# Performance work log

Hardware: AMD Instinct MI355X
Metric: run time of the kernel (lower is better)

## Reference

```python
import jax, jax.numpy as jnp
import numpy as np

KH, KW = 3, 3
STRIDE, PAD = 2, 1
NEG_SLOPE = 0.2
EPS = 1e-5


def conv2d(x, w, stride, pad):
    return jax.lax.conv_general_dilated(
        x, w, window_strides=(stride, stride),
        padding=[(pad, pad), (pad, pad)],
        dimension_numbers=('NCHW', 'OIHW', 'NCHW'))


def deform_conv2d(x, offsets, w_def):
    # x: [B,C,H,W]; offsets: [B,2*K,Ho,Wo] (per-kernel-tap (dy,dx) pairs);
    # w_def: [Cout,Cin,KH,KW]. Matches torchvision DeformConv2d (v1, no mask).
    B, C, H, W = x.shape
    Ho, Wo = offsets.shape[2], offsets.shape[3]
    K = KH * KW
    off = offsets.reshape(B, K, 2, Ho, Wo)
    dy, dx = off[:, :, 0], off[:, :, 1]            # [B,K,Ho,Wo]

    ky = jnp.arange(KH).repeat(KW).astype(x.dtype)   # [K]
    kx = jnp.tile(jnp.arange(KW), KH).astype(x.dtype)
    base_y = (jnp.arange(Ho) * STRIDE - PAD).astype(x.dtype)  # [Ho]
    base_x = (jnp.arange(Wo) * STRIDE - PAD).astype(x.dtype)

    # sampling positions [B,K,Ho,Wo]
    py = base_y[None, None, :, None] + ky[None, :, None, None] + dy
    px = base_x[None, None, None, :] + kx[None, :, None, None] + dx

    y0f = jnp.floor(py); x0f = jnp.floor(px)
    wy1 = py - y0f; wy0 = 1.0 - wy1
    wx1 = px - x0f; wx0 = 1.0 - wx1
    y0 = y0f.astype(jnp.int32); x0 = x0f.astype(jnp.int32)
    y1 = y0 + 1; x1 = x0 + 1

    xt = jnp.transpose(x, (0, 2, 3, 1))  # [B,H,W,C] for channel-last gather
    bidx = jnp.arange(B)[:, None, None, None]

    def corner(yi, xi):
        valid = ((yi >= 0) & (yi < H) & (xi >= 0) & (xi < W)).astype(x.dtype)
        yc = jnp.clip(yi, 0, H - 1); xc = jnp.clip(xi, 0, W - 1)
        v = xt[bidx, yc, xc]                         # [B,K,Ho,Wo,C]
        return v * valid[..., None]

    sampled = (corner(y0, x0) * (wy0 * wx0)[..., None]
               + corner(y0, x1) * (wy0 * wx1)[..., None]
               + corner(y1, x0) * (wy1 * wx0)[..., None]
               + corner(y1, x1) * (wy1 * wx1)[..., None])  # [B,K,Ho,Wo,C]

    wk = w_def.reshape(w_def.shape[0], w_def.shape[1], K)   # [Cout,Cin,K]
    return jnp.einsum('bkhwc,ock->bohw', sampled, wk)


def leaky_relu(x):
    return jnp.where(x >= 0, x, NEG_SLOPE * x)


def instance_norm(x):
    mean = jnp.mean(x, axis=(2, 3), keepdims=True)
    var = jnp.var(x, axis=(2, 3), keepdims=True)
    return (x - mean) * jax.lax.rsqrt(var + EPS)


def setup_inputs() -> dict:
    key = jax.random.key(0)
    k1, k2, k3, k4 = jax.random.split(key, 4)
    B, Cin, H, W = 8, 256, 128, 128
    Cout = 256
    x = jax.random.normal(k1, (B, Cin, H, W), dtype=jnp.float32)
    # conv_offset weight: predicts 2*K offset channels
    w_off = jax.random.normal(k2, (2 * KH * KW, Cin, KH, KW), dtype=jnp.float32) * 0.01
    w_def = jax.random.normal(k3, (Cout, Cin, KH, KW), dtype=jnp.float32) * 0.02
    w_1x1 = jax.random.normal(k4, (Cout, Cout, 1, 1), dtype=jnp.float32) * 0.02
    return {"x": x, "w_off": w_off, "w_def": w_def, "w_1x1": w_1x1}


def reference(x, w_off, w_def, w_1x1):
    offsets = conv2d(x, w_off, STRIDE, PAD)          # [B,18,Ho,Wo]
    y = deform_conv2d(x, offsets, w_def)             # [B,Cout,Ho,Wo]
    y = leaky_relu(y)
    y = conv2d(y, w_1x1, 1, 0)
    y = instance_norm(y)
    return leaky_relu(y)
```

## Files before the change

### kernel.cpp

```cpp
#include <hip/hip_runtime.h>

#define B_   8
#define CIN  256
#define H_   128
#define W_   128
#define HO   64
#define WO   64
#define CO_  256
#define NEG  0.2f

typedef __attribute__((ext_vector_type(8))) _Float16 h16x8;
typedef __attribute__((ext_vector_type(4))) float f32x4;
typedef unsigned short u16;

#define OFF_OFS   0
#define WDEF_OFS  589824
#define W1_OFS    884736
#define WBOFF_OFS 917504
#define Y1_OFS    954368
#define XBF_OFS   5148672
#define TAP_OFS   21925888
#define WS_NEED_TAP ((21925888ull + 1179648ull) * 4ull)

__device__ __forceinline__ float lrelu(float v) { return v >= 0.f ? v : NEG * v; }

__device__ __forceinline__ u16 f2h(float f) {
    _Float16 h = (_Float16)f;
    return *(u16*)&h;
}

__device__ __forceinline__ void gld16(const void* g, void* l) {
    __builtin_amdgcn_global_load_lds((const __attribute__((address_space(1))) unsigned*)g,
                                     (__attribute__((address_space(3))) unsigned*)l, 16, 0, 0);
}

__global__ __launch_bounds__(256) void prep(
    const float* __restrict__ wdef, const float* __restrict__ w1,
    const float* __restrict__ woff,
    u16* __restrict__ wdefh, u16* __restrict__ w1h, u16* __restrict__ wboff)
{
    int i = blockIdx.x * 256 + threadIdx.x;
    if (i < 9 * 256 * 256) {
        int c  = i & 255;
        int co = (i >> 8) & 255;
        int k  = i >> 16;
        wdefh[i] = f2h(wdef[((size_t)co * 256 + c) * 9 + k]);
    }
    if (i < 65536) w1h[i] = f2h(w1[i]);
    if (i < 73728) {
        int j  = i & 7;
        int s  = (i >> 3) & 7;
        int co = (i >> 6) & 31;
        int ch = (i >> 11) & 3;
        int k  = i >> 13;
        int c  = ch * 64 + ((s ^ ((co >> 1) & 7)) << 3) + j;
        wboff[i] = (co < 18) ? f2h(woff[((size_t)co * 256 + c) * 9 + k]) : (u16)0;
    }
}

__global__ __launch_bounds__(256) void nchw2nhwc(
    const float* __restrict__ x, u16* __restrict__ xh)
{
    __shared__ float tile[64][128];
    int bid = blockIdx.x;
    int g = bid & 3;
    int y = (bid >> 2) & 127;
    int b = bid >> 9;
    int t = threadIdx.x;

    const float* src = x + ((size_t)(b * 256 + g * 64) * 128 + y) * 128;
#pragma unroll
    for (int p = 0; p < 8; ++p) {
        int i = p * 256 + t;
        int cc = i >> 5, x4 = (i & 31) * 4;
        *(float4*)&tile[cc][x4] = *(const float4*)(src + (size_t)cc * 16384 + x4);
    }
    __syncthreads();

    int xpos = t >> 1, h = t & 1;
    u16 buf[32];
#pragma unroll
    for (int j = 0; j < 32; ++j) buf[j] = f2h(tile[h * 32 + j][xpos]);
    u16* dst = xh + (((size_t)b * 128 + y) * 128 + xpos) * 256 + g * 64 + h * 32;
#pragma unroll
    for (int q = 0; q < 4; ++q)
        *(int4*)(dst + q * 8) = *(int4*)(buf + q * 8);
}

__global__ __launch_bounds__(256) void offconv_mfma(
    const u16* __restrict__ xh, const u16* __restrict__ wboff,
    float* __restrict__ off, int4* __restrict__ tap)
{
    __shared__ __align__(16) char smem[57728];
    u16* xrowU = (u16*)smem;
    u16* bU    = (u16*)(smem + 49536);

    int blk = blockIdx.x;
    blk = (blk & 7) * 64 + (blk >> 3);
    int b = blk >> 6, ho = blk & 63;
    int t = threadIdx.x;
    int lane = t & 63, w = t >> 6;
    int r = lane & 15, kg = lane >> 4;

    const u16* xB = xh + (size_t)b * (128 * 128 * 256);

    f32x4 acc[2];
    acc[0] = f32x4{0.f, 0.f, 0.f, 0.f};
    acc[1] = f32x4{0.f, 0.f, 0.f, 0.f};

    if (t < 24) {
        int ry = t >> 3, s = t & 7;
        *(int4*)(smem + (ry * 129 * 8 + s) * 16) = int4{0, 0, 0, 0};
    }

    for (int ch = 0; ch < 4; ++ch) {
        __syncthreads();
        for (int ry = 0; ry < 3; ++ry) {
            int y = 2 * ho - 1 + ry;
            int rowbase = (ry * 129 + 1) * 128;
            if ((unsigned)y < 128u) {
#pragma unroll
                for (int p = 0; p < 4; ++p) {
                    int u = p * 256 + t;
                    int xpi = u >> 3, s = u & 7;
                    int c8 = s ^ (((xpi + 1) >> 1) & 7);
                    gld16(xB + ((size_t)(y * 128 + xpi)) * 256 + ch * 64 + c8 * 8,
                          smem + rowbase + p * 4096 + w * 1024);
                }
            } else if (ch == 0) {
#pragma unroll
                for (int p = 0; p < 4; ++p)
                    *(int4*)(smem + rowbase + (p * 256 + t) * 16) = int4{0, 0, 0, 0};
            }
        }
        gld16(wboff + (size_t)(0 * 4 + ch) * 2048 + t * 8,
              smem + 49536 + w * 1024);
        __syncthreads();

        for (int k = 0; k < 9; ++k) {
            int buf = k & 1;
            if (k < 8)
                gld16(wboff + (size_t)((k + 1) * 4 + ch) * 2048 + t * 8,
                      smem + 49536 + (buf ^ 1) * 4096 + w * 1024);
            int ky = k / 3, kx = k - 3 * ky;
            int pixA = w * 16 + r;
            int xp = 2 * pixA + kx;
            int abase = (ky * 129 + xp) * 64;
            int swA = (xp >> 1) & 7;
#pragma unroll
            for (int ksub = 0; ksub < 2; ++ksub) {
                int lc = ksub * 4 + kg;
                h16x8 a = *(h16x8*)(xrowU + abase + ((lc ^ swA) << 3));
#pragma unroll
                for (int n = 0; n < 2; ++n) {
                    int co = n * 16 + r;
                    h16x8 bb = *(h16x8*)(bU + buf * 2048 + co * 64 +
                                         ((lc ^ ((co >> 1) & 7)) << 3));
                    acc[n] = __builtin_amdgcn_mfma_f32_16x16x32_f16(a, bb, acc[n], 0, 0, 0);
                }
            }
            __syncthreads();
        }
    }

    float* offL = (float*)smem;
#pragma unroll
    for (int n = 0; n < 2; ++n) {
        int co = n * 16 + r;
        if (co < 18) {
#pragma unroll
            for (int j = 0; j < 4; ++j) {
                int wo = w * 16 + kg * 4 + j;
                float v = acc[n][j];
                off[(((size_t)b * 18 + co) * 64 + ho) * 64 + wo] = v;
                offL[co * 64 + wo] = v;
            }
        }
    }
    if (tap) {
        __syncthreads();
        for (int i = t; i < 576; i += 256) {
            int pix = i / 9, k = i - 9 * (i / 9);
            int ky = k / 3, kx = k - 3 * ky;
            float dy = offL[(2 * k) * 64 + pix];
            float dx = offL[(2 * k + 1) * 64 + pix];
            float py = (float)(ho * 2 - 1 + ky) + dy;
            float px = (float)(pix * 2 - 1 + kx) + dx;
            float y0f = floorf(py), x0f = floorf(px);
            int y0 = (int)y0f, x0i = (int)x0f;
            float wy1 = py - y0f, wx1 = px - x0f;
            float wy0 = 1.f - wy1, wx0 = 1.f - wx1;
            int y1i = y0 + 1, x1i = x0i + 1;
            bool vy0 = (unsigned)y0  < 128u;
            bool vy1 = (unsigned)y1i < 128u;
            bool vx0 = (unsigned)x0i < 128u;
            bool vx1 = (unsigned)x1i < 128u;
            int yc0 = min(max(y0, 0), 127), yc1 = min(max(y1i, 0), 127);
            int xc0 = min(max(x0i, 0), 127), xc1 = min(max(x1i, 0), 127);
            int4 e;
            e.x = (yc0 * 128 + xc0) * 512 | (xc1 - xc0) | ((yc1 - yc0) << 1);
            e.y = (int)((unsigned)f2h((vy0 && vx0) ? wy0 * wx0 : 0.f) |
                        ((unsigned)f2h((vy0 && vx1) ? wy0 * wx1 : 0.f) << 16));
            e.z = (int)((unsigned)f2h((vy1 && vx0) ? wy1 * wx0 : 0.f) |
                        ((unsigned)f2h((vy1 && vx1) ? wy1 * wx1 : 0.f) << 16));
            e.w = 0;
            tap[(size_t)(b * 64 + ho) * 576 + i] = e;
        }
    }
}

__global__ __launch_bounds__(512, 4) void deform_fused(
    const u16* __restrict__ xh, const int4* __restrict__ tap,
    const u16* __restrict__ wdefh, const u16* __restrict__ w1h,
    float* __restrict__ out)
{
    extern __shared__ __align__(16) char smem[];

    int blk = blockIdx.x;
    blk = (blk & 7) * 64 + (blk >> 3);
    int b = blk >> 6, ho = blk & 63;
    int t = threadIdx.x;
    int lane = t & 63, w = t >> 6;
    int r = lane & 15, kg = lane >> 4;
    int pixS = w * 8 + (lane >> 3);
    int cs   = lane & 7;

    f32x4 acc[4][2];
    f32x4 zz = {0.f, 0.f, 0.f, 0.f};
#pragma unroll
    for (int m = 0; m < 4; ++m)
#pragma unroll
        for (int n = 0; n < 2; ++n) acc[m][n] = zz;

    const int4* tapB = tap + (size_t)(b * 64 + ho) * 576 + pixS * 9;
    const char* xb2  = (const char*)(xh + (size_t)b * (128 * 128 * 256)) + cs * 16;

    int sbw = pixS * 128 + ((cs ^ (pixS & 7)) << 4);

    auto stage = [&](int k, int ch, int dbuf) {
        const u16* wk = wdefh + ((size_t)k << 16);
#pragma unroll
        for (int p2 = 0; p2 < 4; ++p2) {
            int i = p2 * 512 + t;
            int co = i >> 3, s = i & 7;
            gld16(wk + (size_t)co * 256 + ch * 64 + ((s ^ (co & 7)) << 3),
                  smem + dbuf * 32768 + p2 * 8192 + w * 1024);
        }
    };

    {
        stage(0, 0, 0);
        int4 e = tapB[0];
        int o00 = e.x & 0x7FFFFE00;
        int dxo = (e.x & 1) << 9;
        int dyo = (e.x & 2) << 15;
        h16x8 c00 = *(const h16x8*)(xb2 + o00);
        h16x8 c01 = *(const h16x8*)(xb2 + o00 + dxo);
        h16x8 c10 = *(const h16x8*)(xb2 + o00 + dyo);
        h16x8 c11 = *(const h16x8*)(xb2 + o00 + dyo + dxo);
        union U { int u; _Float16 h[2]; };
        U u01, u23;
        u01.u = e.y; u23.u = e.z;
        h16x8 v = c00 * u01.h[0] + c01 * u01.h[1] + c10 * u23.h[0] + c11 * u23.h[1];
        *(h16x8*)(smem + 65536 + sbw) = v;
    }
    __syncthreads();

    for (int p = 0; p < 36; ++p) {
        int cur = p & 1;
        bool nx = p < 35;
        int4 e;
        h16x8 c00, c01, c10, c11;
        if (nx) {
            int pn = p + 1;
            int chn = pn / 9, kn = pn - 9 * chn;
            e = tapB[kn];
            int o00 = e.x & 0x7FFFFE00;
            int dxo = (e.x & 1) << 9;
            int dyo = (e.x & 2) << 15;
            const char* base = xb2 + chn * 128;
            c00 = *(const h16x8*)(base + o00);
            c01 = *(const h16x8*)(base + o00 + dxo);
            c10 = *(const h16x8*)(base + o00 + dyo);
            c11 = *(const h16x8*)(base + o00 + dyo + dxo);
            stage(kn, chn, cur ^ 1);
        }
        {
            u16* wb = (u16*)(smem + cur * 32768);
            u16* sb = (u16*)(smem + 65536 + cur * 8192);
            h16x8 af[4], bfr[2];
            __builtin_amdgcn_s_setprio(1);
#pragma unroll
            for (int ksub = 0; ksub < 2; ++ksub) {
                int so = ((ksub * 4 + kg) ^ (r & 7)) << 3;
#pragma unroll
                for (int m = 0; m < 4; ++m)
                    af[m] = *(h16x8*)(sb + (m * 16 + r) * 64 + so);
#pragma unroll
                for (int n = 0; n < 2; ++n)
                    bfr[n] = *(h16x8*)(wb + (w * 32 + n * 16 + r) * 64 + so);
#pragma unroll
                for (int m = 0; m < 4; ++m)
#pragma unroll
                    for (int n = 0; n < 2; ++n)
                        acc[m][n] = __builtin_amdgcn_mfma_f32_16x16x32_f16(af[m], bfr[n], acc[m][n], 0, 0, 0);
            }
            __builtin_amdgcn_s_setprio(0);
        }
        if (nx) {
            union U { int u; _Float16 h[2]; };
            U u01, u23;
            u01.u = e.y; u23.u = e.z;
            h16x8 v = c00 * u01.h[0] + c01 * u01.h[1] + c10 * u23.h[0] + c11 * u23.h[1];
            *(h16x8*)(smem + 65536 + (cur ^ 1) * 8192 + sbw) = v;
        }
        __syncthreads();
    }

    char* outT = smem + 32768;
    int rg = lane >> 4;
#pragma unroll
    for (int m = 0; m < 4; ++m)
#pragma unroll
        for (int n = 0; n < 2; ++n) {
            int co = w * 32 + n * 16 + r;
#pragma unroll
            for (int j = 0; j < 4; ++j) {
                int prow = m * 16 + rg * 4 + j;
                *(u16*)(outT + prow * 512 + ((co * 2) ^ ((prow & 7) << 4))) =
                    f2h(lrelu(acc[m][n][j]));
            }
        }

    auto stage1 = [&](int ch2) {
#pragma unroll
        for (int p2 = 0; p2 < 4; ++p2) {
            int i = p2 * 512 + t;
            int o = i >> 3, s = i & 7;
            gld16(w1h + (size_t)o * 256 + ch2 * 64 + ((s ^ (o & 7)) << 3),
                  smem + p2 * 8192 + w * 1024);
        }
    };

    stage1(0);
#pragma unroll
    for (int m = 0; m < 4; ++m)
#pragma unroll
        for (int n = 0; n < 2; ++n) acc[m][n] = zz;
    __syncthreads();

    for (int ch2 = 0; ch2 < 4; ++ch2) {
        h16x8 af[4], bfr[2];
        __builtin_amdgcn_s_setprio(1);
#pragma unroll
        for (int ksub = 0; ksub < 2; ++ksub) {
            int cb = (ch2 * 64 + (ksub * 4 + kg) * 8) * 2;
#pragma unroll
            for (int m = 0; m < 4; ++m) {
                int prow = m * 16 + r;
                af[m] = *(h16x8*)(outT + prow * 512 + (cb ^ ((prow & 7) << 4)));
            }
#pragma unroll
            for (int n = 0; n < 2; ++n) {
                int o = w * 32 + n * 16 + r;
                bfr[n] = *(h16x8*)(smem + o * 128 + (((ksub * 4 + kg) ^ (o & 7)) << 4));
            }
#pragma unroll
            for (int m = 0; m < 4; ++m)
#pragma unroll
                for (int n = 0; n < 2; ++n)
                    acc[m][n] = __builtin_amdgcn_mfma_f32_16x16x32_f16(af[m], bfr[n], acc[m][n], 0, 0, 0);
        }
        __builtin_amdgcn_s_setprio(0);
        __syncthreads();
        if (ch2 < 3) {
            stage1(ch2 + 1);
            __syncthreads();
        }
    }

#pragma unroll
    for (int m = 0; m < 4; ++m)
#pragma unroll
        for (int n = 0; n < 2; ++n) {
            int o = w * 32 + n * 16 + r;
            int pix0 = m * 16 + rg * 4;
            float4 v;
            v.x = acc[m][n][0]; v.y = acc[m][n][1];
            v.z = acc[m][n][2]; v.w = acc[m][n][3];
            *(float4*)(out + ((size_t)(b * 256 + o) * 64 + ho) * 64 + pix0) = v;
        }
}

__global__ __launch_bounds__(512, 4) void deform_inline(
    const u16* __restrict__ xh, const float* __restrict__ off,
    const u16* __restrict__ wdefh, u16* __restrict__ y1p)
{
    extern __shared__ __align__(16) char smem[];

    int blk = blockIdx.x;
    blk = (blk & 7) * 64 + (blk >> 3);
    int b = blk >> 6, ho = blk & 63;
    int t = threadIdx.x;
    int lane = t & 63, w = t >> 6;
    int r = lane & 15, kg = lane >> 4;
    int pixS = w * 8 + (lane >> 3);
    int cs   = lane & 7;

    f32x4 acc[4][2];
    f32x4 zz = {0.f, 0.f, 0.f, 0.f};
#pragma unroll
    for (int m = 0; m < 4; ++m)
#pragma unroll
        for (int n = 0; n < 2; ++n) acc[m][n] = zz;

    const u16* xB = xh + (size_t)b * (128 * 128 * 256);

    int o00, o01, o10, o11;
    float f00, f01, f10, f11;

    auto coords = [&](int k) {
        int ky = k / 3, kx = k - 3 * ky;
        float dy = off[(((size_t)b * 18 + 2 * k    ) * 64 + ho) * 64 + pixS];
        float dx = off[(((size_t)b * 18 + 2 * k + 1) * 64 + ho) * 64 + pixS];
        float py = (float)(ho * 2 - 1 + ky) + dy;
        float px = (float)(pixS * 2 - 1 + kx) + dx;
        float y0f = floorf(py), x0f = floorf(px);
        int y0 = (int)y0f, x0i = (int)x0f;
        float wy1 = py - y0f, wx1 = px - x0f;
        float wy0 = 1.f - wy1, wx0 = 1.f - wx1;
        int y1i = y0 + 1, x1i = x0i + 1;
        bool vy0 = (unsigned)y0  < 128u;
        bool vy1 = (unsigned)y1i < 128u;
        bool vx0 = (unsigned)x0i < 128u;
        bool vx1 = (unsigned)x1i < 128u;
        int yc0 = min(max(y0, 0), 127), yc1 = min(max(y1i, 0), 127);
        int xc0 = min(max(x0i, 0), 127), xc1 = min(max(x1i, 0), 127);
        o00 = yc0 * 128 + xc0;  o01 = yc0 * 128 + xc1;
        o10 = yc1 * 128 + xc0;  o11 = yc1 * 128 + xc1;
        f00 = (vy0 && vx0) ? wy0 * wx0 : 0.f;
        f01 = (vy0 && vx1) ? wy0 * wx1 : 0.f;
        f10 = (vy1 && vx0) ? wy1 * wx0 : 0.f;
        f11 = (vy1 && vx1) ? wy1 * wx1 : 0.f;
    };

    auto stage = [&](int k, int ch, int dbuf) {
        const u16* wk = wdefh + ((size_t)k << 16);
#pragma unroll
        for (int p2 = 0; p2 < 4; ++p2) {
            int i = p2 * 512 + t;
            int co = i >> 3, s = i & 7;
            gld16(wk + (size_t)co * 256 + ch * 64 + ((s ^ (co & 7)) << 3),
                  smem + dbuf * 32768 + p2 * 8192 + w * 1024);
        }
    };

    auto sample = [&](int ch, int dbuf) {
        int cw = ch * 64 + cs * 8;
        const u16* q00 = xB + (size_t)o00 * 256 + cw;
        const u16* q01 = xB + (size_t)o01 * 256 + cw;
        const u16* q10 = xB + (size_t)o10 * 256 + cw;
        const u16* q11 = xB + (size_t)o11 * 256 + cw;
        h16x8 c00 = *(const h16x8*)q00;
        h16x8 c01 = *(const h16x8*)q01;
        h16x8 c10 = *(const h16x8*)q10;
        h16x8 c11 = *(const h16x8*)q11;
        _Float16 hf00 = (_Float16)f00, hf01 = (_Float16)f01;
        _Float16 hf10 = (_Float16)f10, hf11 = (_Float16)f11;
        h16x8 v = c00 * hf00 + c01 * hf01 + c10 * hf10 + c11 * hf11;
        *(h16x8*)(smem + 65536 + dbuf * 8192 + pixS * 128 + ((cs ^ (pixS & 7)) << 4)) = v;
    };

    coords(0);
    stage(0, 0, 0);
    sample(0, 0);
    __syncthreads();

    for (int p = 0; p < 36; ++p) {
        int cur = p & 1;
        if (p < 35) {
            int pn = p + 1;
            int chn = pn / 9, kn = pn - 9 * chn;
            stage(kn, chn, cur ^ 1);
            coords(kn);
            sample(chn, cur ^ 1);
        }
        u16* wb = (u16*)(smem + cur * 32768);
        u16* sb = (u16*)(smem + 65536 + cur * 8192);
        h16x8 af[4], bfr[2];
        __builtin_amdgcn_s_setprio(1);
#pragma unroll
        for (int ksub = 0; ksub < 2; ++ksub) {
            int so = ((ksub * 4 + kg) ^ (r & 7)) << 3;
#pragma unroll
            for (int m = 0; m < 4; ++m)
                af[m] = *(h16x8*)(sb + (m * 16 + r) * 64 + so);
#pragma unroll
            for (int n = 0; n < 2; ++n)
                bfr[n] = *(h16x8*)(wb + (w * 32 + n * 16 + r) * 64 + so);
#pragma unroll
            for (int m = 0; m < 4; ++m)
#pragma unroll
                for (int n = 0; n < 2; ++n)
                    acc[m][n] = __builtin_amdgcn_mfma_f32_16x16x32_f16(af[m], bfr[n], acc[m][n], 0, 0, 0);
        }
        __builtin_amdgcn_s_setprio(0);
        __syncthreads();
    }

    u16* outT = (u16*)smem;
    int rg = lane >> 4;
#pragma unroll
    for (int m = 0; m < 4; ++m)
#pragma unroll
        for (int n = 0; n < 2; ++n) {
            int co = w * 32 + n * 16 + r;
#pragma unroll
            for (int j = 0; j < 4; ++j) {
                int prow = m * 16 + rg * 4 + j;
                outT[prow * 256 + co] = f2h(lrelu(acc[m][n][j]));
            }
        }
    __syncthreads();
    u16* dst = y1p + (size_t)(b * 64 + ho) * 16384;
#pragma unroll
    for (int p = 0; p < 4; ++p)
        *(int4*)((char*)dst + p * 8192 + t * 16) = *(int4*)(smem + p * 8192 + t * 16);
}

__global__ __launch_bounds__(256) void conv1x1_mfma(
    const u16* __restrict__ y1p, const u16* __restrict__ w1h,
    float* __restrict__ out)
{
    __shared__ __align__(16) char smem[20480];
    u16* btile = (u16*)smem;
    u16* atile = (u16*)(smem + 16384);

    int blk = blockIdx.x;
    blk = (blk & 7) * 64 + (blk >> 3);
    int b = blk >> 6, ho = blk & 63;
    int t = threadIdx.x, lane = t & 63, w = t >> 6;
    int r = lane & 15, kg = lane >> 4;
    int sR = (r >> 1) & 3;

    f32x4 acc[4][4];
    f32x4 zz = {0.f, 0.f, 0.f, 0.f};
#pragma unroll
    for (int m = 0; m < 4; ++m)
#pragma unroll
        for (int n = 0; n < 4; ++n) acc[m][n] = zz;

    const u16* abase = y1p + (size_t)(b * 64 + ho) * 16384;

    for (int ch = 0; ch < 8; ++ch) {
#pragma unroll
        for (int p = 0; p < 4; ++p) {
            int slot = p * 256 + t;
            int o = slot >> 2, qq = slot & 3;
            gld16(w1h + o * 256 + ch * 32 + ((qq ^ ((o >> 1) & 3)) << 3),
                  smem + p * 4096 + (t >> 6) * 1024);
        }
        {
            int pix = t >> 2, qq = t & 3;
            gld16(abase + pix * 256 + ch * 32 + ((qq ^ ((pix >> 1) & 3)) << 3),
                  smem + 16384 + (t >> 6) * 1024);
        }
        __syncthreads();
        h16x8 af[4], bfr[4];
#pragma unroll
        for (int m = 0; m < 4; ++m)
            af[m] = *(h16x8*)(atile + (m * 16 + r) * 32 + ((kg ^ sR) << 3));
#pragma unroll
        for (int n = 0; n < 4; ++n)
            bfr[n] = *(h16x8*)(btile + (w * 64 + n * 16 + r) * 32 + ((kg ^ sR) << 3));
#pragma unroll
        for (int m = 0; m < 4; ++m)
#pragma unroll
            for (int n = 0; n < 4; ++n)
                acc[m][n] = __builtin_amdgcn_mfma_f32_16x16x32_f16(af[m], bfr[n], acc[m][n], 0, 0, 0);
        __syncthreads();
    }

    int rg = lane >> 4;
#pragma unroll
    for (int m = 0; m < 4; ++m)
#pragma unroll
        for (int n = 0; n < 4; ++n) {
            int o = w * 64 + n * 16 + r;
            int pix0 = m * 16 + rg * 4;
            float4 v;
            v.x = acc[m][n][0]; v.y = acc[m][n][1];
            v.z = acc[m][n][2]; v.w = acc[m][n][3];
            *(float4*)(out + ((size_t)(b * 256 + o) * 64 + ho) * 64 + pix0) = v;
        }
}

__global__ __launch_bounds__(256) void instnorm(float* __restrict__ out)
{
    int bc = blockIdx.x;
    float* p = out + (size_t)bc * 4096;
    int t = threadIdx.x;

    float4 v[4];
    float s1 = 0.f, s2 = 0.f;
#pragma unroll
    for (int i = 0; i < 4; ++i) {
        v[i] = *(const float4*)&p[(t + i * 256) * 4];
        s1 += v[i].x + v[i].y + v[i].z + v[i].w;
        s2 += v[i].x * v[i].x + v[i].y * v[i].y + v[i].z * v[i].z + v[i].w * v[i].w;
    }
#pragma unroll
    for (int o = 32; o > 0; o >>= 1) {
        s1 += __shfl_down(s1, o);
        s2 += __shfl_down(s2, o);
    }
    __shared__ float rs[8];
    __shared__ float mb[2];
    int wave = t >> 6;
    if ((t & 63) == 0) { rs[wave] = s1; rs[4 + wave] = s2; }
    __syncthreads();
    if (t == 0) {
        float a = rs[0] + rs[1] + rs[2] + rs[3];
        float qq = rs[4] + rs[5] + rs[6] + rs[7];
        float mean = a * (1.f / 4096.f);
        float var  = qq * (1.f / 4096.f) - mean * mean;
        mb[0] = mean;
        mb[1] = rsqrtf(var + 1e-5f);
    }
    __syncthreads();
    float mean = mb[0], inv = mb[1];
#pragma unroll
    for (int i = 0; i < 4; ++i) {
        float4 u = v[i];
        u.x = lrelu((u.x - mean) * inv);
        u.y = lrelu((u.y - mean) * inv);
        u.z = lrelu((u.z - mean) * inv);
        u.w = lrelu((u.w - mean) * inv);
        *(float4*)&p[(t + i * 256) * 4] = u;
    }
}

extern "C" void kernel_launch(void* const* d_in, const int* in_sizes, int n_in,
                              void* d_out, int out_size, void* d_ws, size_t ws_size,
                              hipStream_t stream)
{
    const float* x     = (const float*)d_in[0];
    const float* w_off = (const float*)d_in[1];
    const float* w_def = (const float*)d_in[2];
    const float* w1    = (const float*)d_in[3];
    float* out = (float*)d_out;
    float* ws  = (float*)d_ws;

    float* off   = ws + OFF_OFS;
    u16*   wdefh = (u16*)(ws + WDEF_OFS);
    u16*   w1h   = (u16*)(ws + W1_OFS);
    u16*   wboff = (u16*)(ws + WBOFF_OFS);
    u16*   y1p   = (u16*)(ws + Y1_OFS);
    u16*   xh    = (u16*)(ws + XBF_OFS);
    int4*  tap   = (int4*)(ws + TAP_OFS);

    const bool use_tap = ws_size >= WS_NEED_TAP;

    hipFuncSetAttribute((const void*)deform_fused,
                        hipFuncAttributeMaxDynamicSharedMemorySize, 81920);
    hipFuncSetAttribute((const void*)deform_inline,
                        hipFuncAttributeMaxDynamicSharedMemorySize, 81920);

    hipLaunchKernelGGL(prep,         dim3(2304), dim3(256), 0, stream, w_def, w1, w_off, wdefh, w1h, wboff);
    hipLaunchKernelGGL(nchw2nhwc,    dim3(4096), dim3(256), 0, stream, x, xh);
    hipLaunchKernelGGL(offconv_mfma, dim3(512),  dim3(256), 0, stream, xh, wboff, off,
                       use_tap ? tap : (int4*)nullptr);
    if (use_tap) {
        hipLaunchKernelGGL(deform_fused, dim3(512), dim3(512), 81920, stream, xh, tap, wdefh, w1h, out);
    } else {
        hipLaunchKernelGGL(deform_inline, dim3(512), dim3(512), 81920, stream, xh, off, wdefh, y1p);
        hipLaunchKernelGGL(conv1x1_mfma,  dim3(512), dim3(256), 0, stream, y1p, w1h, out);
    }
    hipLaunchKernelGGL(instnorm,     dim3(2048), dim3(256), 0, stream, out);
}
```

Measured before the change: 144.8 us.

## Load deform weights straight into registers instead of staging through LDS

In the fused deformable-conv kernel, the per-tap weight tile is no longer copied into shared memory with async global-to-LDS loads. Each lane now loads its MFMA B-fragments directly from global memory into double-buffered registers, and the loop is unrolled by two to alternate register sets. This removes the LDS weight buffers and cuts dynamic shared memory from 80KB to 64KB, which may allow more blocks per CU. The cost is more global/L2 traffic, since weights are read per wave rather than once per block, plus extra register pressure.

Result: slower. 178.2 us (+23.1%).

```diff
diff --git a/kernel.cpp b/kernel.cpp
--- a/kernel.cpp
+++ b/kernel.cpp
@@ -234,22 +234,42 @@
 
     const int4* tapB = tap + (size_t)(b * 64 + ho) * 576 + pixS * 9;
     const char* xb2  = (const char*)(xh + (size_t)b * (128 * 128 * 256)) + cs * 16;
+    const u16* wlane = wdefh + (size_t)(w * 32 + r) * 256 + kg * 8;
 
     int sbw = pixS * 128 + ((cs ^ (pixS & 7)) << 4);
 
-    auto stage = [&](int k, int ch, int dbuf) {
-        const u16* wk = wdefh + ((size_t)k << 16);
-#pragma unroll
-        for (int p2 = 0; p2 < 4; ++p2) {
-            int i = p2 * 512 + t;
-            int co = i >> 3, s = i & 7;
-            gld16(wk + (size_t)co * 256 + ch * 64 + ((s ^ (co & 7)) << 3),
-                  smem + dbuf * 32768 + p2 * 8192 + w * 1024);
-        }
+    auto loadW = [&](int p, h16x8 (&dst)[2][2]) {
+        int ch = p / 9, k = p - 9 * ch;
+        const u16* wp = wlane + ((size_t)k << 16) + ch * 64;
+#pragma unroll
+        for (int ks = 0; ks < 2; ++ks)
+#pragma unroll
+            for (int n = 0; n < 2; ++n)
+                dst[ks][n] = *(const h16x8*)(wp + n * 16 * 256 + ks * 32);
     };
 
+    auto mfmaPhase = [&](h16x8 (&wreg)[2][2], char* sbc) {
+        u16* sb = (u16*)sbc;
+        h16x8 af[4];
+        __builtin_amdgcn_s_setprio(1);
+#pragma unroll
+        for (int ks = 0; ks < 2; ++ks) {
+            int so = ((ks * 4 + kg) ^ (r & 7)) << 3;
+#pragma unroll
+            for (int m = 0; m < 4; ++m)
+                af[m] = *(h16x8*)(sb + (m * 16 + r) * 64 + so);
+#pragma unroll
+            for (int m = 0; m < 4; ++m)
+#pragma unroll
+                for (int n = 0; n < 2; ++n)
+                    acc[m][n] = __builtin_amdgcn_mfma_f32_16x16x32_f16(af[m], wreg[ks][n], acc[m][n], 0, 0, 0);
+        }
+        __builtin_amdgcn_s_setprio(0);
+    };
+
+    h16x8 wA[2][2], wB[2][2];
+
     {
-        stage(0, 0, 0);
         int4 e = tapB[0];
         int o00 = e.x & 0x7FFFFE00;
         int dxo = (e.x & 1) << 9;
@@ -258,61 +278,58 @@
         h16x8 c01 = *(const h16x8*)(xb2 + o00 + dxo);
         h16x8 c10 = *(const h16x8*)(xb2 + o00 + dyo);
         h16x8 c11 = *(const h16x8*)(xb2 + o00 + dyo + dxo);
+        loadW(0, wA);
         union U { int u; _Float16 h[2]; };
         U u01, u23;
         u01.u = e.y; u23.u = e.z;
         h16x8 v = c00 * u01.h[0] + c01 * u01.h[1] + c10 * u23.h[0] + c11 * u23.h[1];
-        *(h16x8*)(smem + 65536 + sbw) = v;
+        *(h16x8*)(smem + sbw) = v;
     }
     __syncthreads();
 
-    for (int p = 0; p < 36; ++p) {
-        int cur = p & 1;
-        bool nx = p < 35;
-        int4 e;
-        h16x8 c00, c01, c10, c11;
-        if (nx) {
-            int pn = p + 1;
-            int chn = pn / 9, kn = pn - 9 * chn;
-            e = tapB[kn];
+    for (int pp = 0; pp < 36; pp += 2) {
+        {
+            int pn = pp + 1;
+            int kn = pn - 9 * (pn / 9), chn = pn / 9;
+            int4 e = tapB[kn];
             int o00 = e.x & 0x7FFFFE00;
             int dxo = (e.x & 1) << 9;
             int dyo = (e.x & 2) << 15;
             const char* base = xb2 + chn * 128;
-            c00 = *(const h16x8*)(base + o00);
-            c01 = *(const h16x8*)(base + o00 + dxo);
-            c10 = *(const h16x8*)(base + o00 + dyo);
-            c11 = *(const h16x8*)(base + o00 + dyo + dxo);
-            stage(kn, chn, cur ^ 1);
-        }
-        {
-            u16* wb = (u16*)(smem + cur * 32768);
-            u16* sb = (u16*)(smem + 65536 + cur * 8192);
-            h16x8 af[4], bfr[2];
-            __builtin_amdgcn_s_setprio(1);
-#pragma unroll
-            for (int ksub = 0; ksub < 2; ++ksub) {
-                int so = ((ksub * 4 + kg) ^ (r & 7)) << 3;
-#pragma unroll
-                for (int m = 0; m < 4; ++m)
-                    af[m] = *(h16x8*)(sb + (m * 16 + r) * 64 + so);
-#pragma unroll
-                for (int n = 0; n < 2; ++n)
-                    bfr[n] = *(h16x8*)(wb + (w * 32 + n * 16 + r) * 64 + so);
-#pragma unroll
-                for (int m = 0; m < 4; ++m)
-#pragma unroll
-                    for (int n = 0; n < 2; ++n)
-                        acc[m][n] = __builtin_amdgcn_mfma_f32_16x16x32_f16(af[m], bfr[n], acc[m][n], 0, 0, 0);
-            }
-            __builtin_amdgcn_s_setprio(0);
-        }
-        if (nx) {
+            h16x8 c00 = *(const h16x8*)(base + o00);
+            h16x8 c01 = *(const h16x8*)(base + o00 + dxo);
+            h16x8 c10 = *(const h16x8*)(base + o00 + dyo);
+            h16x8 c11 = *(const h16x8*)(base + o00 + dyo + dxo);
+            loadW(pn, wB);
+            mfmaPhase(wA, smem);
             union U { int u; _Float16 h[2]; };
             U u01, u23;
             u01.u = e.y; u23.u = e.z;
             h16x8 v = c00 * u01.h[0] + c01 * u01.h[1] + c10 * u23.h[0] + c11 * u23.h[1];
-            *(h16x8*)(smem + 65536 + (cur ^ 1) * 8192 + sbw) = v;
+            *(h16x8*)(smem + 8192 + sbw) = v;
+        }
+        __syncthreads();
+        if (pp + 2 < 36) {
+            int pn = pp + 2;
+            int kn = pn - 9 * (pn / 9), chn = pn / 9;
+            int4 e = tapB[kn];
+            int o00 = e.x & 0x7FFFFE00;
+            int dxo = (e.x & 1) << 9;
+            int dyo = (e.x & 2) << 15;
+            const char* base = xb2 + chn * 128;
+            h16x8 c00 = *(const h16x8*)(base + o00);
+            h16x8 c01 = *(const h16x8*)(base + o00 + dxo);
+            h16x8 c10 = *(const h16x8*)(base + o00 + dyo);
+            h16x8 c11 = *(const h16x8*)(base + o00 + dyo + dxo);
+            loadW(pn, wA);
+            mfmaPhase(wB, smem + 8192);
+            union U { int u; _Float16 h[2]; };
+            U u01, u23;
+            u01.u = e.y; u23.u = e.z;
+            h16x8 v = c00 * u01.h[0] + c01 * u01.h[1] + c10 * u23.h[0] + c11 * u23.h[1];
+            *(h16x8*)(smem + sbw) = v;
+        } else {
+            mfmaPhase(wB, smem + 8192);
         }
         __syncthreads();
     }
@@ -662,7 +679,7 @@
     const bool use_tap = ws_size >= WS_NEED_TAP;
 
     hipFuncSetAttribute((const void*)deform_fused,
-                        hipFuncAttributeMaxDynamicSharedMemorySize, 81920);
+                        hipFuncAttributeMaxDynamicSharedMemorySize, 65536);
     hipFuncSetAttribute((const void*)deform_inline,
                         hipFuncAttributeMaxDynamicSharedMemorySize, 81920);
 
@@ -671,7 +688,7 @@
     hipLaunchKernelGGL(offconv_mfma, dim3(512),  dim3(256), 0, stream, xh, wboff, off,
                        use_tap ? tap : (int4*)nullptr);
     if (use_tap) {
-        hipLaunchKernelGGL(deform_fused, dim3(512), dim3(512), 81920, stream, xh, tap, wdefh, w1h, out);
+        hipLaunchKernelGGL(deform_fused, dim3(512), dim3(512), 65536, stream, xh, tap, wdefh, w1h, out);
     } else {
         hipLaunchKernelGGL(deform_inline, dim3(512), dim3(512), 81920, stream, xh, off, wdefh, y1p);
         hipLaunchKernelGGL(conv1x1_mfma,  dim3(512), dim3(256), 0, stream, y1p, w1h, out);
```
